# Optimization experiments

Measured on AMD Instinct MI355X. Metric: run time of the kernel, lower is better.

## Reference

```python
import jax, jax.numpy as jnp
import numpy as np

DIM = 2048
NUM_HEADS = 16
HEAD_DIM = DIM // NUM_HEADS  # 128
ROPE_BASE = 10000.0


def setup_inputs() -> dict:
    key = jax.random.key(0)
    k1, k2, k3 = jax.random.split(key, 3)
    B, S = 2, 2048
    x = jax.random.normal(k1, (B, S, DIM), dtype=jnp.float32)
    # causal mask: 1 where allowed (k <= q), 0 elsewhere
    mask = jnp.tril(jnp.ones((S, S), dtype=jnp.int32))
    # torch Linear(dim, 3*dim, bias=False): store transposed so y = x @ w
    w_qkv = jax.random.normal(k2, (DIM, 3 * DIM), dtype=jnp.float32) / np.sqrt(DIM)
    w_out = jax.random.normal(k3, (DIM, DIM), dtype=jnp.float32) / np.sqrt(DIM)
    return {"x": x, "w_qkv": w_qkv, "w_out": w_out, "mask": mask}


def _rope_cos_sin(seq_len, dtype):
    inv_freq = 1.0 / (ROPE_BASE ** (jnp.arange(0, HEAD_DIM, 2, dtype=jnp.float32) / HEAD_DIM))
    t = jnp.arange(seq_len, dtype=jnp.float32)
    freqs = t[:, None] * inv_freq[None, :]          # [S, D/2]
    emb = jnp.concatenate([freqs, freqs], axis=-1)  # [S, D]
    return jnp.cos(emb).astype(dtype), jnp.sin(emb).astype(dtype)


def _rotate_half(x):
    x1, x2 = jnp.split(x, 2, axis=-1)
    return jnp.concatenate([-x2, x1], axis=-1)


def reference(x, w_qkv, w_out, mask):
    B, S, _ = x.shape
    H, D = NUM_HEADS, HEAD_DIM
    qkv = x @ w_qkv                                   # [B, S, 3*dim]
    qkv = qkv.reshape(B, S, 3, H, D).transpose(2, 0, 3, 1, 4)  # [3, B, H, S, D]
    q, k, v = qkv[0], qkv[1], qkv[2]
    cos, sin = _rope_cos_sin(S, x.dtype)              # [S, D] broadcast over B,H
    q = q * cos + _rotate_half(q) * sin
    k = k * cos + _rotate_half(k) * sin
    scale = D ** -0.5
    score = jnp.einsum("bhqd,bhkd->bhqk", q, k) * scale
    score = jnp.where(mask == 0, -jnp.inf, score)
    attn = jax.nn.softmax(score, axis=-1)             # dropout = identity (eval)
    out = jnp.einsum("bhqk,bhkd->bhqd", attn, v)
    out = out.transpose(0, 2, 1, 3).reshape(B, S, H * D)
    return out @ w_out
```

## Files before the change

### kernel.cpp

```cpp
#include <hip/hip_runtime.h>

typedef __attribute__((ext_vector_type(8))) __bf16 bf16x8;
typedef __attribute__((ext_vector_type(4))) float f32x4;

__device__ __forceinline__ unsigned short f2bf(float x) {
  union { float f; unsigned int u; } v; v.f = x;
  unsigned int r = v.u + 0x7fffu + ((v.u >> 16) & 1u);
  return (unsigned short)(r >> 16);
}
__device__ __forceinline__ float bf2f(unsigned short x) {
  union { unsigned int u; float f; } v; v.u = ((unsigned int)x) << 16;
  return v.f;
}
__device__ __forceinline__ void g2l16(const void* g, void* l) {
  __builtin_amdgcn_global_load_lds((const __attribute__((address_space(1))) void*)g,
                                   (__attribute__((address_space(3))) void*)l, 16, 0, 0);
}

#define BARX()                                  \
  do {                                          \
    asm volatile("" ::: "memory");              \
    __builtin_amdgcn_s_barrier();               \
    asm volatile("" ::: "memory");              \
  } while (0)

__global__ __launch_bounds__(256) void prep_k(const float* __restrict__ x,
                                              const float* __restrict__ wq,
                                              const float* __restrict__ wo,
                                              unsigned short* __restrict__ xb,
                                              unsigned short* __restrict__ wqT,
                                              unsigned short* __restrict__ woT) {
  __shared__ unsigned short t[64][65];
  const int b = blockIdx.x;
  if (b < 8192) {
    int i = b * 256 + threadIdx.x;
    float4 v = ((const float4*)x)[i];
    ushort4 o;
    o.x = f2bf(v.x); o.y = f2bf(v.y); o.z = f2bf(v.z); o.w = f2bf(v.w);
    ((ushort4*)xb)[i] = o;
    return;
  }
  const float* in; unsigned short* out; int C, c0, r0;
  const int R = 2048;
  if (b < 11264) { int bb = b - 8192;  in = wq; out = wqT; C = 6144; c0 = (bb % 96) * 64; r0 = (bb / 96) * 64; }
  else           { int bb = b - 11264; in = wo; out = woT; C = 2048; c0 = (bb & 31) * 64; r0 = (bb >> 5) * 64; }
  const int tx = threadIdx.x & 63, tg = threadIdx.x >> 6;
#pragma unroll
  for (int i = 0; i < 16; i++) {
    int r = i * 4 + tg;
    t[r][tx] = f2bf(in[(size_t)(r0 + r) * C + c0 + tx]);
  }
  __syncthreads();
#pragma unroll
  for (int i = 0; i < 16; i++) {
    int c = i * 4 + tg;
    out[(size_t)(c0 + c) * R + r0 + tx] = t[tx][c];
  }
}

__global__ __launch_bounds__(512) void gemm8_qkv(const unsigned short* __restrict__ A,
                                                 const unsigned short* __restrict__ BT,
                                                 unsigned short* __restrict__ oq,
                                                 unsigned short* __restrict__ ok,
                                                 unsigned short* __restrict__ ov) {
  __shared__ __align__(16) unsigned short smem8[65536];
  const int tid = threadIdx.x;
  const int w = tid >> 6, lane = tid & 63;
  const int quad = lane >> 4, l16 = lane & 15;
  const int id = (int)blockIdx.x;
  const int wg = (id & 7) * 48 + (id >> 3);
  const int bx = wg % 24, by = wg / 24;
  const int m0 = by * 256, n0 = bx * 256;
  const int wm = (w >> 2) * 128, wn = (w & 3) * 64;
  f32x4 acc[8][4] = {};

  const int rr = tid >> 3, csw = (tid & 7) ^ (rr & 7);
  const unsigned short* gA = A + (size_t)(m0 + rr) * 2048 + csw * 8;
  const unsigned short* gB = BT + (size_t)(n0 + rr) * 2048 + csw * 8;
  char* ldst = (char*)smem8 + tid * 16;
  auto STAGE = [&](int s) {
    if (s <= 127) {
      const int tau = s >> 2, u = s & 3, hh = u & 1;
      char* l = ldst + ((u < 2) ? 65536 : 0) + (tau & 1) * 32768 + hh * 16384;
      const unsigned short* g = ((u < 2) ? gB : gA) + (size_t)hh * 128 * 2048 + tau * 64;
      g2l16(g, (void*)l);
      g2l16(g + (size_t)64 * 2048, (void*)(l + 8192));
    }
  };

  const char* sA = (const char*)smem8 + (wm >> 7) * 16384 + l16 * 128;
  const char* sB = (const char*)smem8 + 65536 + (wn >> 7) * 16384 + ((wn & 64) + l16) * 128;
  const int x0 = (quad ^ (l16 & 7)) * 16;
  const int x1 = ((4 + quad) ^ (l16 & 7)) * 16;

#define KTILE(T, PB, NV)                                                                          \
  {                                                                                               \
    bf16x8 a0[4][2], a1[4][2], b0[2][2], b1[2][2];                                                \
    _Pragma("unroll") for (int i = 0; i < 4; ++i) {                                               \
      a0[i][0] = *(const bf16x8*)(sA + (PB) + i * 2048 + x0);                                     \
      a0[i][1] = *(const bf16x8*)(sA + (PB) + i * 2048 + x1);                                     \
    }                                                                                             \
    _Pragma("unroll") for (int j = 0; j < 2; ++j) {                                               \
      b0[j][0] = *(const bf16x8*)(sB + (PB) + j * 2048 + x0);                                     \
      b0[j][1] = *(const bf16x8*)(sB + (PB) + j * 2048 + x1);                                     \
    }                                                                                             \
    STAGE(4 * (T) + 7);                                                                           \
    BARX();                                                                                       \
    asm volatile("s_waitcnt lgkmcnt(0)" ::: "memory");                                            \
    __builtin_amdgcn_s_setprio(1);                                                                \
    _Pragma("unroll") for (int ks = 0; ks < 2; ++ks)                                              \
      _Pragma("unroll") for (int i = 0; i < 4; ++i)                                               \
        _Pragma("unroll") for (int j = 0; j < 2; ++j)                                             \
          acc[i][j] = __builtin_amdgcn_mfma_f32_16x16x32_bf16(a0[i][ks], b0[j][ks], acc[i][j], 0, 0, 0); \
    __builtin_amdgcn_s_setprio(0);                                                                \
    BARX();                                                                                       \
    _Pragma("unroll") for (int j = 0; j < 2; ++j) {                                               \
      b1[j][0] = *(const bf16x8*)(sB + (PB) + (j + 2) * 2048 + x0);                               \
      b1[j][1] = *(const bf16x8*)(sB + (PB) + (j + 2) * 2048 + x1);                               \
    }                                                                                             \
    STAGE(4 * (T) + 8);                                                                           \
    BARX();                                                                                       \
    asm volatile("s_waitcnt lgkmcnt(0)" ::: "memory");                                            \
    __builtin_amdgcn_s_setprio(1);                                                                \
    _Pragma("unroll") for (int ks = 0; ks < 2; ++ks)                                              \
      _Pragma("unroll") for (int i = 0; i < 4; ++i)                                               \
        _Pragma("unroll") for (int j = 0; j < 2; ++j)                                             \
          acc[i][j + 2] = __builtin_amdgcn_mfma_f32_16x16x32_bf16(a0[i][ks], b1[j][ks], acc[i][j + 2], 0, 0, 0); \
    __builtin_amdgcn_s_setprio(0);                                                                \
    BARX();                                                                                       \
    _Pragma("unroll") for (int i = 0; i < 4; ++i) {                                               \
      a1[i][0] = *(const bf16x8*)(sA + (PB) + (i + 4) * 2048 + x0);                               \
      a1[i][1] = *(const bf16x8*)(sA + (PB) + (i + 4) * 2048 + x1);                               \
    }                                                                                             \
    STAGE(4 * (T) + 9);                                                                           \
    BARX();                                                                                       \
    asm volatile("s_waitcnt lgkmcnt(0)" ::: "memory");                                            \
    __builtin_amdgcn_s_setprio(1);                                                                \
    _Pragma("unroll") for (int ks = 0; ks < 2; ++ks)                                              \
      _Pragma("unroll") for (int i = 0; i < 4; ++i)                                               \
        _Pragma("unroll") for (int j = 0; j < 2; ++j)                                             \
          acc[i + 4][j] = __builtin_amdgcn_mfma_f32_16x16x32_bf16(a1[i][ks], b0[j][ks], acc[i + 4][j], 0, 0, 0); \
    __builtin_amdgcn_s_setprio(0);                                                                \
    BARX();                                                                                       \
    STAGE(4 * (T) + 10);                                                                          \
    BARX();                                                                                       \
    __builtin_amdgcn_s_setprio(1);                                                                \
    _Pragma("unroll") for (int ks = 0; ks < 2; ++ks)                                              \
      _Pragma("unroll") for (int i = 0; i < 4; ++i)                                               \
        _Pragma("unroll") for (int j = 0; j < 2; ++j)                                             \
          acc[i + 4][j + 2] = __builtin_amdgcn_mfma_f32_16x16x32_bf16(a1[i][ks], b1[j][ks], acc[i + 4][j + 2], 0, 0, 0); \
    __builtin_amdgcn_s_setprio(0);                                                                \
    if ((NV) == 6) asm volatile("s_waitcnt vmcnt(6)" ::: "memory");                               \
    else if ((NV) == 0) asm volatile("s_waitcnt vmcnt(0)" ::: "memory");                          \
    BARX();                                                                                       \
  }

  for (int s = 0; s < 7; ++s) STAGE(s);
  asm volatile("s_waitcnt vmcnt(6)" ::: "memory");
  BARX();

  for (int t2 = 0; t2 < 32; t2 += 2) {
    KTILE(t2, 0, (t2 == 30) ? 0 : 6);
    KTILE(t2 + 1, 32768, (t2 + 1 == 31) ? -1 : 6);
  }
#undef KTILE

  const int which = n0 >> 11;
  const int h2 = (n0 >> 7) & 15;
  const int bi2 = m0 >> 11, s0 = m0 & 2047;
  if (which < 2) {
    unsigned short* dst = which ? ok : oq;
    const float scale = which ? 1.0f : 0.08838834764831845f;
    const int d = tid & 63, tg = (tid >> 6) & 3, rh = tid >> 8;
    const float fr = exp2f(-(float)d * (13.287712379549449f / 64.0f));
    for (int ch = 0; ch < 2; ++ch) {
      BARX();
      if (((w >> 1) & 1) == ch) {
        const int rw = w >> 2, cl = (w & 1) * 64;
#pragma unroll
        for (int i = 0; i < 8; ++i)
#pragma unroll
          for (int r = 0; r < 4; ++r) {
            int row = i * 16 + quad * 4 + r;
#pragma unroll
            for (int j = 0; j < 4; ++j)
              smem8[rw * 16640 + row * 130 + cl + j * 16 + l16] = f2bf(acc[i][j][r]);
          }
      }
      BARX();
      const int h = (h2 + ch) & 15;
      const size_t hb = ((size_t)(bi2 * 16 + h) * 2048 + s0 + rh * 128) * 128;
      const unsigned short* tl = smem8 + rh * 16640;
#pragma unroll
      for (int i = 0; i < 32; ++i) {
        int r = i * 4 + tg;
        float xa = bf2f(tl[r * 130 + d]);
        float xb2 = bf2f(tl[r * 130 + 64 + d]);
        float sn, cs;
        __sincosf((float)(s0 + rh * 128 + r) * fr, &sn, &cs);
        dst[hb + (size_t)r * 128 + d]      = f2bf((xa * cs - xb2 * sn) * scale);
        dst[hb + (size_t)r * 128 + 64 + d] = f2bf((xb2 * cs + xa * sn) * scale);
      }
    }
  } else {
    const int sc = tid & 15, dbase = (tid >> 4) & 15, rh = tid >> 8;
    for (int ch = 0; ch < 2; ++ch) {
      BARX();
      if (((w >> 1) & 1) == ch) {
        const int rw = w >> 2, cl = (w & 1) * 64;
#pragma unroll
        for (int i = 0; i < 8; ++i)
#pragma unroll
          for (int j = 0; j < 4; ++j) {
            int row = i * 16 + quad * 4;
            int col = cl + j * 16 + l16;
            ushort4 t4;
            t4.x = f2bf(acc[i][j][0]); t4.y = f2bf(acc[i][j][1]);
            t4.z = f2bf(acc[i][j][2]); t4.w = f2bf(acc[i][j][3]);
            *(ushort4*)&smem8[rw * 17408 + col * 136 + row] = t4;
          }
      }
      BARX();
      const int h = (h2 + ch) & 15;
      const size_t vrb = ((size_t)(bi2 * 16 + h) * 128) * 2048 + s0 + rh * 128;
#pragma unroll
      for (int vv = 0; vv < 8; ++vv) {
        int dd = dbase + vv * 16;
        uint4 val = *(const uint4*)&smem8[rh * 17408 + dd * 136 + sc * 8];
        *(uint4*)(ov + vrb + (size_t)dd * 2048 + sc * 8) = val;
      }
    }
  }
}

template <int EPI>
__global__ __launch_bounds__(256) void gemm_bt_k(const unsigned short* __restrict__ A,
                                                 const unsigned short* __restrict__ BT,
                                                 int K, int N,
                                                 float* __restrict__ outF,
                                                 unsigned short* __restrict__ oq,
                                                 unsigned short* __restrict__ ok,
                                                 unsigned short* __restrict__ ov) {
  __shared__ __align__(16) unsigned short smem[17408];
  unsigned short* lA = smem;
  unsigned short* lB = smem + 8192;
  const int tid = threadIdx.x;
  const int w = tid >> 6, lane = tid & 63;
  const int quad = lane >> 4, l16 = lane & 15;
  const int m0 = blockIdx.y * 128, n0 = blockIdx.x * 128;
  const int wm = (w >> 1) * 64, wn = (w & 1) * 64;
  f32x4 acc[4][4] = {};
  const int srow = tid >> 3;
  const int schunk = (tid & 7) ^ (srow & 7);
  const unsigned short* gA = A + (size_t)(m0 + srow) * K + schunk * 8;
  const unsigned short* gB = BT + (size_t)(n0 + srow) * K + schunk * 8;
  char* ldA = (char*)lA + tid * 16;
  char* ldB = (char*)lB + tid * 16;
  const size_t rskip = (size_t)32 * K;
  for (int k0 = 0; k0 < K; k0 += 64) {
#pragma unroll
    for (int j = 0; j < 4; j++) {
      g2l16(gA + k0 + j * rskip, ldA + j * 4096);
      g2l16(gB + k0 + j * rskip, ldB + j * 4096);
    }
    __syncthreads();
#pragma unroll
    for (int ks = 0; ks < 2; ks++) {
      bf16x8 af[4], bfv[4];
#pragma unroll
      for (int i = 0; i < 4; i++)
        af[i] = *(const bf16x8*)((const char*)lA + (size_t)(wm + i * 16 + l16) * 128 +
                                 ((size_t)((ks * 4 + quad) ^ (l16 & 7)) * 16));
#pragma unroll
      for (int j = 0; j < 4; j++)
        bfv[j] = *(const bf16x8*)((const char*)lB + (size_t)(wn + j * 16 + l16) * 128 +
                                  ((size_t)((ks * 4 + quad) ^ (l16 & 7)) * 16));
#pragma unroll
      for (int i = 0; i < 4; i++)
#pragma unroll
        for (int j = 0; j < 4; j++)
          acc[i][j] = __builtin_amdgcn_mfma_f32_16x16x32_bf16(af[i], bfv[j], acc[i][j], 0, 0, 0);
    }
    __syncthreads();
  }
  if (EPI == 1) {
#pragma unroll
    for (int i = 0; i < 4; i++)
#pragma unroll
      for (int r = 0; r < 4; r++) {
        size_t rowb = (size_t)(m0 + wm + i * 16 + quad * 4 + r) * N;
#pragma unroll
        for (int j = 0; j < 4; j++)
          outF[rowb + n0 + wn + j * 16 + l16] = acc[i][j][r];
      }
  }
}

__global__ __launch_bounds__(256, 2) void attn_k(const unsigned short* __restrict__ qb,
                                                 const unsigned short* __restrict__ kb,
                                                 const unsigned short* __restrict__ vt,
                                                 unsigned short* __restrict__ ob) {
  __shared__ __align__(16) unsigned short lK[64 * 128];
  __shared__ __align__(16) unsigned short lV[128 * 64];
  __shared__ __align__(16) __bf16 pbuf[4][32 * 72];
  const int tid = threadIdx.x;
  const int w = tid >> 6, lane = tid & 63;
  const int quad = lane >> 4, l16 = lane & 15;
  const int qt = (blockIdx.y < 16) ? (int)blockIdx.x : 15 - (int)blockIdx.x;
  const int bh = blockIdx.y;
  const int bi = bh >> 4, h = bh & 15;
  const int q0w = qt * 128 + w * 32;
  const unsigned short* qp = qb + (size_t)bh * 2048 * 128;
  const unsigned short* kp = kb + (size_t)bh * 2048 * 128;
  const unsigned short* vp = vt + (size_t)bh * 128 * 2048;
  __bf16* pw = pbuf[w];

  bf16x8 qf[2][4];
#pragma unroll
  for (int rg = 0; rg < 2; rg++) {
    const unsigned short* qr = qp + (size_t)(q0w + rg * 16 + l16) * 128 + quad * 8;
#pragma unroll
    for (int st = 0; st < 4; st++) qf[rg][st] = *(const bf16x8*)(qr + st * 32);
  }
  f32x4 o[2][8] = {};
  f32x4 lsum[2] = {};

  const int krow = tid >> 4;
  const int kcg = (tid & 15) ^ krow;
  const int vd = tid >> 3;
  const int vsg = (tid & 7) ^ ((tid >> 3) & 7);
  unsigned short* lKdst = lK + (size_t)tid * 8;
  unsigned short* lVdst = lV + (size_t)tid * 8;

  const int nkt = 2 * qt + 2;
  const int myNkt = (q0w + 31) / 64 + 1;
  for (int kt = 0; kt < nkt; kt++) {
    const int kt0 = kt * 64;
#pragma unroll
    for (int j = 0; j < 4; j++) {
      g2l16(kp + (size_t)(kt0 + j * 16 + krow) * 128 + kcg * 8, lKdst + j * 2048);
      g2l16(vp + (size_t)(j * 32 + vd) * 2048 + kt0 + vsg * 8, lVdst + j * 2048);
    }
    __syncthreads();
    if (kt < myNkt) {
      f32x4 sc[2][4] = {};
#pragma unroll
      for (int ct = 0; ct < 4; ct++) {
        const int nrow = ct * 16 + l16;
#pragma unroll
        for (int st = 0; st < 4; st++) {
          bf16x8 kf = *(const bf16x8*)(lK + ((size_t)nrow * 16 + ((st * 4 + quad) ^ l16)) * 8);
          sc[0][ct] = __builtin_amdgcn_mfma_f32_16x16x32_bf16(qf[0][st], kf, sc[0][ct], 0, 0, 0);
          sc[1][ct] = __builtin_amdgcn_mfma_f32_16x16x32_bf16(qf[1][st], kf, sc[1][ct], 0, 0, 0);
        }
      }
      const bool needmask = (kt == myNkt - 1);
#pragma unroll
      for (int rg = 0; rg < 2; rg++)
#pragma unroll
        for (int ct = 0; ct < 4; ct++) {
          const int col = kt0 + ct * 16 + l16;
          const int rowb = q0w + rg * 16 + quad * 4;
#pragma unroll
          for (int r = 0; r < 4; r++) {
            float s = sc[rg][ct][r];
            if (needmask && col > rowb + r) s = -1e30f;
            float e = __expf(s);
            lsum[rg][r] += e;
            pw[(rg * 16 + quad * 4 + r) * 72 + ct * 16 + l16] = (__bf16)e;
          }
        }
      bf16x8 pf[2][2];
#pragma unroll
      for (int rg = 0; rg < 2; rg++)
#pragma unroll
        for (int sb = 0; sb < 2; sb++)
          pf[rg][sb] = *(const bf16x8*)(pw + (rg * 16 + l16) * 72 + sb * 32 + quad * 8);
#pragma unroll
      for (int dt = 0; dt < 8; dt++) {
#pragma unroll
        for (int sb = 0; sb < 2; sb++) {
          bf16x8 vf = *(const bf16x8*)(lV +
              ((size_t)(dt * 16 + l16) * 8 + ((sb * 4 + quad) ^ (l16 & 7))) * 8);
          o[0][dt] = __builtin_amdgcn_mfma_f32_16x16x32_bf16(pf[0][sb], vf, o[0][dt], 0, 0, 0);
          o[1][dt] = __builtin_amdgcn_mfma_f32_16x16x32_bf16(pf[1][sb], vf, o[1][dt], 0, 0, 0);
        }
      }
    }
    __syncthreads();
  }
#pragma unroll
  for (int m = 1; m < 16; m <<= 1)
#pragma unroll
    for (int rg = 0; rg < 2; rg++)
#pragma unroll
      for (int r = 0; r < 4; r++)
        lsum[rg][r] += __shfl_xor(lsum[rg][r], m, 64);
  float inv[2][4];
#pragma unroll
  for (int rg = 0; rg < 2; rg++)
#pragma unroll
    for (int r = 0; r < 4; r++) inv[rg][r] = 1.0f / lsum[rg][r];
#pragma unroll
  for (int rg = 0; rg < 2; rg++)
#pragma unroll
    for (int dt = 0; dt < 8; dt++)
#pragma unroll
      for (int r = 0; r < 4; r++)
        ob[(size_t)(bi * 2048 + q0w + rg * 16 + quad * 4 + r) * 2048 + h * 128 + dt * 16 + l16] =
            f2bf(o[rg][dt][r] * inv[rg][r]);
}

extern "C" void kernel_launch(void* const* d_in, const int* in_sizes, int n_in,
                              void* d_out, int out_size, void* d_ws, size_t ws_size,
                              hipStream_t stream) {
  const float* x = (const float*)d_in[0];
  const float* wqkv = (const float*)d_in[1];
  const float* wout = (const float*)d_in[2];
  char* ws = (char*)d_ws;
  const size_t MiB = 1ull << 20;
  unsigned short* xb    = (unsigned short*)(ws + 0);
  unsigned short* wqkvT = (unsigned short*)(ws + 16 * MiB);
  unsigned short* woutT = (unsigned short*)(ws + 40 * MiB);
  unsigned short* qb    = (unsigned short*)(ws + 48 * MiB);
  unsigned short* kb    = (unsigned short*)(ws + 64 * MiB);
  unsigned short* vtb   = (unsigned short*)(ws + 80 * MiB);
  unsigned short* attnb = (unsigned short*)(ws + 96 * MiB);
  float* outF = (float*)d_out;

  prep_k<<<12288, 256, 0, stream>>>(x, wqkv, wout, xb, wqkvT, woutT);
  gemm8_qkv<<<384, 512, 0, stream>>>(xb, wqkvT, qb, kb, vtb);
  attn_k<<<dim3(16, 32), 256, 0, stream>>>(qb, kb, vtb, attnb);
  gemm_bt_k<1><<<dim3(16, 32), 256, 0, stream>>>(attnb, woutT, 2048, 2048, outF,
                                                 nullptr, nullptr, nullptr);
}
```

Before: 428.7 us.

## Split RoPE and V transpose out of QKV GEMM epilogue into separate kernel

The QKV GEMM epilogue now writes raw bf16 Q/K/V straight to per-head global layout without the LDS staging. A new rt_k kernel applies RoPE and scaling in place to Q/K and transposes V through shared memory. The GEMM also gets a min-blocks hint of 2 and moves one K-stage prefetch later. This drops LDS round-trips and barriers from the GEMM tail, at the cost of an extra launch and another global read/write pass over Q/K/V.

```diff
diff --git a/kernel.cpp b/kernel.cpp
--- a/kernel.cpp
+++ b/kernel.cpp
@@ -58,11 +58,11 @@
   }
 }
 
-__global__ __launch_bounds__(512) void gemm8_qkv(const unsigned short* __restrict__ A,
-                                                 const unsigned short* __restrict__ BT,
-                                                 unsigned short* __restrict__ oq,
-                                                 unsigned short* __restrict__ ok,
-                                                 unsigned short* __restrict__ ov) {
+__global__ __launch_bounds__(512, 2) void gemm8_qkv(const unsigned short* __restrict__ A,
+                                                    const unsigned short* __restrict__ BT,
+                                                    unsigned short* __restrict__ oq,
+                                                    unsigned short* __restrict__ ok,
+                                                    unsigned short* __restrict__ ovr) {
   __shared__ __align__(16) unsigned short smem8[65536];
   const int tid = threadIdx.x;
   const int w = tid >> 6, lane = tid & 63;
@@ -118,7 +118,6 @@
       b1[j][0] = *(const bf16x8*)(sB + (PB) + (j + 2) * 2048 + x0);                               \
       b1[j][1] = *(const bf16x8*)(sB + (PB) + (j + 2) * 2048 + x1);                               \
     }                                                                                             \
-    STAGE(4 * (T) + 8);                                                                           \
     BARX();                                                                                       \
     asm volatile("s_waitcnt lgkmcnt(0)" ::: "memory");                                            \
     __builtin_amdgcn_s_setprio(1);                                                                \
@@ -132,6 +131,7 @@
       a1[i][0] = *(const bf16x8*)(sA + (PB) + (i + 4) * 2048 + x0);                               \
       a1[i][1] = *(const bf16x8*)(sA + (PB) + (i + 4) * 2048 + x1);                               \
     }                                                                                             \
+    STAGE(4 * (T) + 8);                                                                           \
     STAGE(4 * (T) + 9);                                                                           \
     BARX();                                                                                       \
     asm volatile("s_waitcnt lgkmcnt(0)" ::: "memory");                                            \
@@ -166,70 +166,67 @@
 #undef KTILE
 
   const int which = n0 >> 11;
-  const int h2 = (n0 >> 7) & 15;
+  unsigned short* dst = (which == 0) ? oq : (which == 1 ? ok : ovr);
   const int bi2 = m0 >> 11, s0 = m0 & 2047;
-  if (which < 2) {
-    unsigned short* dst = which ? ok : oq;
+  const int n0h = (n0 >> 7) & 15;
+#pragma unroll
+  for (int i = 0; i < 8; ++i)
+#pragma unroll
+    for (int r = 0; r < 4; ++r) {
+      const int s = s0 + wm + i * 16 + quad * 4 + r;
+      const size_t rowb = ((size_t)(bi2 * 16) * 2048 + s) * 128;
+#pragma unroll
+      for (int j = 0; j < 4; ++j) {
+        const int c = wn + j * 16 + l16;
+        dst[rowb + (size_t)(n0h + (c >> 7)) * 262144 + (c & 127)] = f2bf(acc[i][j][r]);
+      }
+    }
+}
+
+__global__ __launch_bounds__(256) void rt_k(unsigned short* __restrict__ qb,
+                                            unsigned short* __restrict__ kb,
+                                            const unsigned short* __restrict__ vr,
+                                            unsigned short* __restrict__ vt) {
+  const int b = blockIdx.x;
+  const int tid = threadIdx.x;
+  if (b < 1024) {
+    const int which = b >> 9, bh = (b >> 4) & 31, sc = b & 15;
+    unsigned short* p = (which ? kb : qb) + (size_t)bh * 262144 + sc * 16384;
     const float scale = which ? 1.0f : 0.08838834764831845f;
-    const int d = tid & 63, tg = (tid >> 6) & 3, rh = tid >> 8;
+    const int d = tid & 63, tg = tid >> 6;
     const float fr = exp2f(-(float)d * (13.287712379549449f / 64.0f));
-    for (int ch = 0; ch < 2; ++ch) {
-      BARX();
-      if (((w >> 1) & 1) == ch) {
-        const int rw = w >> 2, cl = (w & 1) * 64;
-#pragma unroll
-        for (int i = 0; i < 8; ++i)
-#pragma unroll
-          for (int r = 0; r < 4; ++r) {
-            int row = i * 16 + quad * 4 + r;
-#pragma unroll
-            for (int j = 0; j < 4; ++j)
-              smem8[rw * 16640 + row * 130 + cl + j * 16 + l16] = f2bf(acc[i][j][r]);
-          }
-      }
-      BARX();
-      const int h = (h2 + ch) & 15;
-      const size_t hb = ((size_t)(bi2 * 16 + h) * 2048 + s0 + rh * 128) * 128;
-      const unsigned short* tl = smem8 + rh * 16640;
-#pragma unroll
-      for (int i = 0; i < 32; ++i) {
-        int r = i * 4 + tg;
-        float xa = bf2f(tl[r * 130 + d]);
-        float xb2 = bf2f(tl[r * 130 + 64 + d]);
-        float sn, cs;
-        __sincosf((float)(s0 + rh * 128 + r) * fr, &sn, &cs);
-        dst[hb + (size_t)r * 128 + d]      = f2bf((xa * cs - xb2 * sn) * scale);
-        dst[hb + (size_t)r * 128 + 64 + d] = f2bf((xb2 * cs + xa * sn) * scale);
-      }
-    }
-  } else {
-    const int sc = tid & 15, dbase = (tid >> 4) & 15, rh = tid >> 8;
-    for (int ch = 0; ch < 2; ++ch) {
-      BARX();
-      if (((w >> 1) & 1) == ch) {
-        const int rw = w >> 2, cl = (w & 1) * 64;
-#pragma unroll
-        for (int i = 0; i < 8; ++i)
-#pragma unroll
-          for (int j = 0; j < 4; ++j) {
-            int row = i * 16 + quad * 4;
-            int col = cl + j * 16 + l16;
-            ushort4 t4;
-            t4.x = f2bf(acc[i][j][0]); t4.y = f2bf(acc[i][j][1]);
-            t4.z = f2bf(acc[i][j][2]); t4.w = f2bf(acc[i][j][3]);
-            *(ushort4*)&smem8[rw * 17408 + col * 136 + row] = t4;
-          }
-      }
-      BARX();
-      const int h = (h2 + ch) & 15;
-      const size_t vrb = ((size_t)(bi2 * 16 + h) * 128) * 2048 + s0 + rh * 128;
-#pragma unroll
-      for (int vv = 0; vv < 8; ++vv) {
-        int dd = dbase + vv * 16;
-        uint4 val = *(const uint4*)&smem8[rh * 17408 + dd * 136 + sc * 8];
-        *(uint4*)(ov + vrb + (size_t)dd * 2048 + sc * 8) = val;
-      }
-    }
+#pragma unroll
+    for (int i = 0; i < 32; ++i) {
+      const int r = i * 4 + tg;
+      float a = bf2f(p[r * 128 + d]);
+      float bb = bf2f(p[r * 128 + 64 + d]);
+      float sn, cs;
+      __sincosf((float)(sc * 128 + r) * fr, &sn, &cs);
+      p[r * 128 + d]      = f2bf((a * cs - bb * sn) * scale);
+      p[r * 128 + 64 + d] = f2bf((bb * cs + a * sn) * scale);
+    }
+    return;
+  }
+  __shared__ unsigned short t[64][65];
+  const int bb = b - 1024, bh = bb >> 4, sc = bb & 15;
+  const unsigned short* src = vr + (size_t)bh * 262144 + sc * 16384;
+  unsigned short* dst = vt + (size_t)bh * 262144 + sc * 128;
+  const int tx = tid & 63, tg = tid >> 6;
+#pragma unroll
+  for (int q4 = 0; q4 < 4; ++q4) {
+    const int sy = q4 >> 1, dx = q4 & 1;
+#pragma unroll
+    for (int i = 0; i < 16; ++i) {
+      const int r = i * 4 + tg;
+      t[r][tx] = src[(size_t)(sy * 64 + r) * 128 + dx * 64 + tx];
+    }
+    __syncthreads();
+#pragma unroll
+    for (int i = 0; i < 16; ++i) {
+      const int c = i * 4 + tg;
+      dst[(size_t)(dx * 64 + c) * 2048 + sy * 64 + tx] = t[tx][c];
+    }
+    __syncthreads();
   }
 }
 
@@ -237,10 +234,7 @@
 __global__ __launch_bounds__(256) void gemm_bt_k(const unsigned short* __restrict__ A,
                                                  const unsigned short* __restrict__ BT,
                                                  int K, int N,
-                                                 float* __restrict__ outF,
-                                                 unsigned short* __restrict__ oq,
-                                                 unsigned short* __restrict__ ok,
-                                                 unsigned short* __restrict__ ov) {
+                                                 float* __restrict__ outF) {
   __shared__ __align__(16) unsigned short smem[17408];
   unsigned short* lA = smem;
   unsigned short* lB = smem + 8192;
@@ -283,17 +277,15 @@
     }
     __syncthreads();
   }
-  if (EPI == 1) {
-#pragma unroll
-    for (int i = 0; i < 4; i++)
-#pragma unroll
-      for (int r = 0; r < 4; r++) {
-        size_t rowb = (size_t)(m0 + wm + i * 16 + quad * 4 + r) * N;
-#pragma unroll
-        for (int j = 0; j < 4; j++)
-          outF[rowb + n0 + wn + j * 16 + l16] = acc[i][j][r];
-      }
-  }
+#pragma unroll
+  for (int i = 0; i < 4; i++)
+#pragma unroll
+    for (int r = 0; r < 4; r++) {
+      size_t rowb = (size_t)(m0 + wm + i * 16 + quad * 4 + r) * N;
+#pragma unroll
+      for (int j = 0; j < 4; j++)
+        outF[rowb + n0 + wn + j * 16 + l16] = acc[i][j][r];
+    }
 }
 
 __global__ __launch_bounds__(256, 2) void attn_k(const unsigned short* __restrict__ qb,
@@ -429,8 +421,8 @@
   float* outF = (float*)d_out;
 
   prep_k<<<12288, 256, 0, stream>>>(x, wqkv, wout, xb, wqkvT, woutT);
-  gemm8_qkv<<<384, 512, 0, stream>>>(xb, wqkvT, qb, kb, vtb);
+  gemm8_qkv<<<384, 512, 0, stream>>>(xb, wqkvT, qb, kb, attnb);
+  rt_k<<<1536, 256, 0, stream>>>(qb, kb, attnb, vtb);
   attn_k<<<dim3(16, 32), 256, 0, stream>>>(qb, kb, vtb, attnb);
-  gemm_bt_k<1><<<dim3(16, 32), 256, 0, stream>>>(attnb, woutT, 2048, 2048, outF,
-                                                 nullptr, nullptr, nullptr);
-}
+  gemm_bt_k<1><<<dim3(16, 32), 256, 0, stream>>>(attnb, woutT, 2048, 2048, outF);
+}
```

Result: faster. 394.2 us (-8.0%).
